# Optimization experiments

Measured on AMD Instinct MI355X. Metric: run time of the kernel, lower is better.

## Reference

```python
import jax, jax.numpy as jnp
import numpy as np

NUM_HEADS = 16


def setup_inputs() -> dict:
    key = jax.random.key(0)
    k1, k2, k3 = jax.random.split(key, 3)
    x = jax.random.normal(k1, (2, 2048, 1024), dtype=jnp.float32)
    w_qkv = jax.random.normal(k2, (3072, 1024), dtype=jnp.float32) * 0.02
    b_qkv = jax.random.normal(k3, (3072,), dtype=jnp.float32) * 0.02
    return {"x": x, "w_qkv": w_qkv, "b_qkv": b_qkv}


def reference(x, w_qkv, b_qkv):
    b, s, _ = x.shape
    d_model = w_qkv.shape[0] // 3
    head_dim = d_model // NUM_HEADS
    # fused QKV projection (torch Linear: x @ W^T + b)
    qkv = x @ w_qkv.T + b_qkv                      # [b, s, 3*d_model]
    qkv = qkv.reshape(b, s, NUM_HEADS, 3 * head_dim)
    qkv = jnp.transpose(qkv, (0, 2, 1, 3))          # [b, h, s, 3*hd]
    q, k, v = jnp.split(qkv, 3, axis=-1)            # each [b, h, s, hd]
    scale = 1.0 / np.sqrt(head_dim).astype(np.float32)
    scores = jnp.einsum("bhqd,bhkd->bhqk", q, k) * scale
    attn = jax.nn.softmax(scores, axis=-1)
    values = jnp.einsum("bhqk,bhkd->bhqd", attn, v)  # [b, h, s, hd]
    # Faithful to source: reshape WITHOUT permuting heads back (head-interleaved)
    return values.reshape(b, s, d_model)
```

## Files before the change

### kernel.cpp

```cpp
#include <hip/hip_runtime.h>
#include <cstdint>

typedef unsigned short ushort_t;

#define M_ROWS 4096
#define N_COLS 3072
#define K_DIM  1024
#define S_LEN  2048
#define NHEADS 16
#define HDIM   64
#define QSCALE 0.1803368801111204f

typedef __bf16 bf16_t;
typedef bf16_t  bf16x8  __attribute__((ext_vector_type(8)));
typedef short   shortx4 __attribute__((ext_vector_type(4)));
typedef float   floatx4 __attribute__((ext_vector_type(4)));
typedef ushort_t ushortx4 __attribute__((ext_vector_type(4)));

union U32x2S4 { unsigned u[2]; shortx4 s; };

__device__ __forceinline__ unsigned short f2bf(float f) {
  unsigned u = __float_as_uint(f);
  u += 0x7FFFu + ((u >> 16) & 1u);
  return (unsigned short)(u >> 16);
}

__device__ __forceinline__ unsigned pkbf(float a, float b) {
  unsigned ua = __float_as_uint(a) + 0x8000u;
  unsigned ub = __float_as_uint(b) + 0x8000u;
  return __builtin_amdgcn_perm(ub, ua, 0x07060302u);
}

__device__ __forceinline__ unsigned cvtpk(float a, float b) {
#if __has_builtin(__builtin_amdgcn_cvt_pk_bf16_f32)
  auto t = __builtin_amdgcn_cvt_pk_bf16_f32(a, b);
  unsigned r;
  __builtin_memcpy(&r, &t, 4);
  return r;
#else
  return pkbf(a, b);
#endif
}

__device__ __forceinline__ float fexp2(float x) {
#if __has_builtin(__builtin_amdgcn_exp2f)
  return __builtin_amdgcn_exp2f(x);
#else
  float r; asm volatile("v_exp_f32 %0, %1\n\ts_nop 1" : "=v"(r) : "v"(x)); return r;
#endif
}

__device__ __forceinline__ void gload_lds16(const void* g, void* l) {
  __builtin_amdgcn_global_load_lds(
      (const __attribute__((address_space(1))) unsigned int*)g,
      (__attribute__((address_space(3))) unsigned int*)l,
      16, 0, 0);
}

__global__ __launch_bounds__(256) void cvt_bf16_kernel(
    const float* __restrict__ x, const float* __restrict__ w,
    ushort_t* __restrict__ Xb, ushort_t* __restrict__ Wb) {
  const int NX8 = (M_ROWS * K_DIM) / 8;
  int i = blockIdx.x * 256 + threadIdx.x;
  const float4* src;
  ushort_t* dst;
  int idx;
  if (i < NX8) { src = (const float4*)x; dst = Xb; idx = i; }
  else         { src = (const float4*)w; dst = Wb; idx = i - NX8; }
  float4 a = src[2 * idx];
  float4 b = src[2 * idx + 1];
  uint4 o;
  o.x = cvtpk(a.x, a.y);
  o.y = cvtpk(a.z, a.w);
  o.z = cvtpk(b.x, b.y);
  o.w = cvtpk(b.z, b.w);
  *(uint4*)(dst + 8 * (size_t)idx) = o;
}

__global__ __launch_bounds__(256) void qkv_gemm_kernel(
    const ushort_t* __restrict__ Xb, const ushort_t* __restrict__ Wb,
    const float* __restrict__ bias,
    ushort_t* __restrict__ Qb, ushort_t* __restrict__ Kb, ushort_t* __restrict__ Vb) {
  __shared__ ushort_t As[128 * 64];
  __shared__ ushort_t Bs[128 * 64];
  const int tid = threadIdx.x;
  const int l = tid & 63, w = tid >> 6;
  const int quad = l >> 4, lj = l & 15;
  const int m0 = blockIdx.y * 128, n0 = blockIdx.x * 128;
  const int wm = (w & 1) * 64, wn = (w >> 1) * 64;

  floatx4 acc[4][4] = {};

  const int srow = w * 32 + (l >> 3);
  const int scol = ((l & 7) ^ (l >> 3)) * 8;
  const ushort_t* gA = Xb + (size_t)(m0 + srow) * K_DIM + scol;
  const ushort_t* gB = Wb + (size_t)(n0 + srow) * K_DIM + scol;
  ushort_t* lA = As + (w * 32) * 64;
  ushort_t* lB = Bs + (w * 32) * 64;

  const int swr = lj & 7;

  for (int k0 = 0; k0 < K_DIM; k0 += 64) {
    __syncthreads();
#pragma unroll
    for (int c = 0; c < 4; ++c) {
      gload_lds16(gA + (size_t)(c * 8) * K_DIM + k0, lA + c * 8 * 64);
      gload_lds16(gB + (size_t)(c * 8) * K_DIM + k0, lB + c * 8 * 64);
    }
    __syncthreads();
#pragma unroll
    for (int kk = 0; kk < 2; ++kk) {
      const int ch = ((kk * 4 + quad) ^ swr) * 8;
      bf16x8 aF[4], bF[4];
#pragma unroll
      for (int i = 0; i < 4; ++i)
        aF[i] = *(const bf16x8*)(As + (wm + i * 16 + lj) * 64 + ch);
#pragma unroll
      for (int j = 0; j < 4; ++j)
        bF[j] = *(const bf16x8*)(Bs + (wn + j * 16 + lj) * 64 + ch);
#pragma unroll
      for (int i = 0; i < 4; ++i)
#pragma unroll
        for (int j = 0; j < 4; ++j)
          acc[i][j] = __builtin_amdgcn_mfma_f32_16x16x32_bf16(aF[i], bF[j], acc[i][j], 0, 0, 0);
    }
  }

#pragma unroll
  for (int j = 0; j < 4; ++j) {
    const int n = n0 + wn + j * 16 + lj;
    const int h = n / 192;
    const int r = n - h * 192;
    const int seg = r >> 6;
    const int d = r & 63;
    const float bv = bias[n];
    ushort_t* dst = (seg == 0) ? Qb : (seg == 1) ? Kb : Vb;
    const float scl = (seg == 0) ? QSCALE : 1.0f;
    const size_t base = (size_t)h * S_LEN * HDIM + d;
#pragma unroll
    for (int i = 0; i < 4; ++i) {
#pragma unroll
      for (int rg = 0; rg < 4; ++rg) {
        const int m = m0 + wm + i * 16 + quad * 4 + rg;
        const int bi = m >> 11;
        const int si = m & 2047;
        dst[base + ((size_t)bi * NHEADS * S_LEN + si) * HDIM] =
            f2bf((acc[i][j][rg] + bv) * scl);
      }
    }
  }
}

__global__ __launch_bounds__(512, 4) void attn_kernel(
    const ushort_t* __restrict__ Qb, const ushort_t* __restrict__ Kb,
    const ushort_t* __restrict__ Vb, float* __restrict__ out) {
  __shared__ ushort_t Ks[128 * 64];
  __shared__ ushort_t Vs[64 * 140];
  const int tid = threadIdx.x;
  const int l = tid & 63, w = tid >> 6;
  const int quad = l >> 4, lj = l & 15;
  const int bh = blockIdx.x >> 4;
  const int qt = blockIdx.x & 15;
  const int q0 = qt * 128 + w * 16;
  const size_t headoff = (size_t)bh * S_LEN * HDIM;

  bf16x8 qF[2];
#pragma unroll
  for (int kk = 0; kk < 2; ++kk)
    qF[kk] = *(const bf16x8*)(Qb + headoff + (size_t)(q0 + lj) * HDIM +
                              kk * 32 + quad * 8);

  floatx4 accO[4] = {};
  float l_runA = 0.f, l_runB = 0.f;

  const int kr = tid >> 3;
  const int kc = ((tid & 7) ^ (kr & 7)) * 8;
  const ushort_t* gK = Kb + headoff + (size_t)kr * HDIM + kc;
  ushort_t* lK = Ks + tid * 8;

  const int dq = tid & 15;
  const int spw = tid >> 4;
  const ushort_t* gV = Vb + headoff + dq * 4;
  unsigned* Vs32 = (unsigned*)Vs;
  const int swz = (dq >> 2) << 1;

  const int swk = lj & 7;

  for (int kb = 0; kb < 16; ++kb) {
    const int kv0 = kb * 128;
    __syncthreads();
#pragma unroll
    for (int c = 0; c < 2; ++c)
      gload_lds16(gK + (size_t)(kv0 + c * 64) * HDIM, lK + c * 64 * 64);
#pragma unroll
    for (int R = 0; R < 2; ++R) {
      const int sp = R * 32 + spw;
      const ushort_t* g = gV + (size_t)(kv0 + 2 * sp) * HDIM;
      const uint2 v0 = *(const uint2*)g;
      const uint2 v1 = *(const uint2*)(g + HDIM);
      unsigned o0 = __builtin_amdgcn_perm(v1.x, v0.x, 0x05040100u);
      unsigned o1 = __builtin_amdgcn_perm(v1.x, v0.x, 0x07060302u);
      unsigned o2 = __builtin_amdgcn_perm(v1.y, v0.y, 0x05040100u);
      unsigned o3 = __builtin_amdgcn_perm(v1.y, v0.y, 0x07060302u);
      const int sp2 = sp ^ swz;
      Vs32[(4 * dq + 0) * 70 + sp2] = o0;
      Vs32[(4 * dq + 1) * 70 + sp2] = o1;
      Vs32[(4 * dq + 2) * 70 + sp2] = o2;
      Vs32[(4 * dq + 3) * 70 + sp2] = o3;
    }
    __syncthreads();

    floatx4 accST[8];
#pragma unroll
    for (int c = 0; c < 8; ++c) {
      const ushort_t* krow = Ks + (c * 16 + lj) * 64;
      bf16x8 kF0 = *(const bf16x8*)(krow + ((quad ^ swk) * 8));
      bf16x8 kF1 = *(const bf16x8*)(krow + (((quad ^ swk) ^ 4) * 8));
      floatx4 z = {0.f, 0.f, 0.f, 0.f};
      z = __builtin_amdgcn_mfma_f32_16x16x32_bf16(kF0, qF[0], z, 0, 0, 0);
      accST[c] = __builtin_amdgcn_mfma_f32_16x16x32_bf16(kF1, qF[1], z, 0, 0, 0);
    }

    shortx4 aP[8];
    float lsA = 0.f, lsB = 0.f;
#pragma unroll
    for (int c = 0; c < 8; ++c) {
      float p0 = fexp2(accST[c][0]);
      float p1 = fexp2(accST[c][1]);
      float p2 = fexp2(accST[c][2]);
      float p3 = fexp2(accST[c][3]);
      lsA += p0 + p1;
      lsB += p2 + p3;
      U32x2S4 t;
      t.u[0] = cvtpk(p0, p1);
      t.u[1] = cvtpk(p2, p3);
      aP[c] = t.s;
    }
    l_runA += lsA;
    l_runB += lsB;

#pragma unroll
    for (int dt = 0; dt < 4; ++dt) {
      const ushort_t* vp = Vs + (dt * 16 + lj) * 140 + (quad ^ dt) * 4;
#pragma unroll
      for (int c = 0; c < 8; ++c) {
        shortx4 vF = *(const shortx4*)(vp + c * 16);
        accO[dt] = __builtin_amdgcn_mfma_f32_16x16x16bf16_1k(aP[c], vF, accO[dt], 0, 0, 0);
      }
    }
  }

  {
    float ls = l_runA + l_runB;
    ls += __shfl_xor(ls, 16, 64);
    ls += __shfl_xor(ls, 32, 64);
    const float inv = 1.0f / ls;
    const int sbase = (l & 48) | (quad * 4);
    float iv[4];
    iv[0] = __shfl(inv, sbase + 0, 64);
    iv[1] = __shfl(inv, sbase + 1, 64);
    iv[2] = __shfl(inv, sbase + 2, 64);
    iv[3] = __shfl(inv, sbase + 3, 64);
#pragma unroll
    for (int dt = 0; dt < 4; ++dt) {
#pragma unroll
      for (int rg = 0; rg < 4; ++rg) {
        const int q = q0 + quad * 4 + rg;
        out[headoff + (size_t)q * HDIM + dt * 16 + lj] = accO[dt][rg] * iv[rg];
      }
    }
  }
}

extern "C" void kernel_launch(void* const* d_in, const int* in_sizes, int n_in,
                              void* d_out, int out_size, void* d_ws, size_t ws_size,
                              hipStream_t stream) {
  (void)in_sizes; (void)n_in; (void)out_size; (void)ws_size;
  const float* x  = (const float*)d_in[0];
  const float* wq = (const float*)d_in[1];
  const float* bq = (const float*)d_in[2];
  float* out = (float*)d_out;

  char* ws = (char*)d_ws;
  ushort_t* Qb = (ushort_t*)(ws);
  ushort_t* Kb = (ushort_t*)(ws + 8388608);
  ushort_t* Vb = (ushort_t*)(ws + 16777216);
  ushort_t* Xb = (ushort_t*)(ws + 25165824);
  ushort_t* Wb = (ushort_t*)(ws + 33554432);

  cvt_bf16_kernel<<<3584, 256, 0, stream>>>(x, wq, Xb, Wb);
  qkv_gemm_kernel<<<dim3(N_COLS / 128, M_ROWS / 128), 256, 0, stream>>>(Xb, Wb, bq, Qb, Kb, Vb);
  attn_kernel<<<512, 512, 0, stream>>>(Qb, Kb, Vb, out);
}
```

Baseline: 162.3 us.

## Load K fragments directly from global and remap block order for L2 locality

The attention kernel no longer stages K tiles in shared memory. Each lane loads its K fragments straight from global memory into registers, and the QK^T MFMA is fused with the exp/pack loop. The barrier now sits after the score computation, so the V stores to LDS overlap with the K loads and MFMAs. Block indices are also permuted so consecutive blocks land on different heads/q-tiles, which changes L2 reuse. In exchange, each of the 8 waves fetches K redundantly from global/L2 instead of once per block, which adds cache traffic.

```diff
diff --git a/kernel.cpp b/kernel.cpp
--- a/kernel.cpp
+++ b/kernel.cpp
@@ -154,13 +154,13 @@
 __global__ __launch_bounds__(512, 4) void attn_kernel(
     const ushort_t* __restrict__ Qb, const ushort_t* __restrict__ Kb,
     const ushort_t* __restrict__ Vb, float* __restrict__ out) {
-  __shared__ ushort_t Ks[128 * 64];
   __shared__ ushort_t Vs[64 * 140];
   const int tid = threadIdx.x;
   const int l = tid & 63, w = tid >> 6;
   const int quad = l >> 4, lj = l & 15;
-  const int bh = blockIdx.x >> 4;
-  const int qt = blockIdx.x & 15;
+  const int id = (blockIdx.x & 7) * 64 + (blockIdx.x >> 3);
+  const int bh = id >> 4;
+  const int qt = id & 15;
   const int q0 = qt * 128 + w * 16;
   const size_t headoff = (size_t)bh * S_LEN * HDIM;
 
@@ -172,11 +172,6 @@
 
   floatx4 accO[4] = {};
   float l_runA = 0.f, l_runB = 0.f;
-
-  const int kr = tid >> 3;
-  const int kc = ((tid & 7) ^ (kr & 7)) * 8;
-  const ushort_t* gK = Kb + headoff + (size_t)kr * HDIM + kc;
-  ushort_t* lK = Ks + tid * 8;
 
   const int dq = tid & 15;
   const int spw = tid >> 4;
@@ -184,14 +179,12 @@
   unsigned* Vs32 = (unsigned*)Vs;
   const int swz = (dq >> 2) << 1;
 
-  const int swk = lj & 7;
+  const ushort_t* gK = Kb + headoff + (size_t)lj * HDIM + quad * 8;
 
   for (int kb = 0; kb < 16; ++kb) {
     const int kv0 = kb * 128;
     __syncthreads();
-#pragma unroll
-    for (int c = 0; c < 2; ++c)
-      gload_lds16(gK + (size_t)(kv0 + c * 64) * HDIM, lK + c * 64 * 64);
+
 #pragma unroll
     for (int R = 0; R < 2; ++R) {
       const int sp = R * 32 + spw;
@@ -208,27 +201,22 @@
       Vs32[(4 * dq + 2) * 70 + sp2] = o2;
       Vs32[(4 * dq + 3) * 70 + sp2] = o3;
     }
-    __syncthreads();
-
-    floatx4 accST[8];
+
+    shortx4 aP[8];
+    float lsA = 0.f, lsB = 0.f;
+    const ushort_t* gKt = gK + (size_t)kv0 * HDIM;
 #pragma unroll
     for (int c = 0; c < 8; ++c) {
-      const ushort_t* krow = Ks + (c * 16 + lj) * 64;
-      bf16x8 kF0 = *(const bf16x8*)(krow + ((quad ^ swk) * 8));
-      bf16x8 kF1 = *(const bf16x8*)(krow + (((quad ^ swk) ^ 4) * 8));
+      const ushort_t* krow = gKt + (size_t)(c * 16) * HDIM;
+      bf16x8 kF0 = *(const bf16x8*)(krow);
+      bf16x8 kF1 = *(const bf16x8*)(krow + 32);
       floatx4 z = {0.f, 0.f, 0.f, 0.f};
       z = __builtin_amdgcn_mfma_f32_16x16x32_bf16(kF0, qF[0], z, 0, 0, 0);
-      accST[c] = __builtin_amdgcn_mfma_f32_16x16x32_bf16(kF1, qF[1], z, 0, 0, 0);
-    }
-
-    shortx4 aP[8];
-    float lsA = 0.f, lsB = 0.f;
-#pragma unroll
-    for (int c = 0; c < 8; ++c) {
-      float p0 = fexp2(accST[c][0]);
-      float p1 = fexp2(accST[c][1]);
-      float p2 = fexp2(accST[c][2]);
-      float p3 = fexp2(accST[c][3]);
+      floatx4 st = __builtin_amdgcn_mfma_f32_16x16x32_bf16(kF1, qF[1], z, 0, 0, 0);
+      float p0 = fexp2(st[0]);
+      float p1 = fexp2(st[1]);
+      float p2 = fexp2(st[2]);
+      float p3 = fexp2(st[3]);
       lsA += p0 + p1;
       lsB += p2 + p3;
       U32x2S4 t;
@@ -238,6 +226,7 @@
     }
     l_runA += lsA;
     l_runB += lsB;
+    __syncthreads();
 
 #pragma unroll
     for (int dt = 0; dt < 4; ++dt) {
```

Measured after the change: 240.6 us. 1.48x slower.

## Split attention KV range across two wave halves with LDS merge, double grid

Applied to the files above, without the earlier changes.

Each block now handles 64 query rows instead of 128. Its two halves of four waves each process opposite halves of the KV sequence, and the partial outputs and row sums are merged through LDS at the end. The grid doubles to 1024 blocks and is remapped so consecutive blocks spread across heads, which raises parallelism and may improve L2 locality. In exchange, each KV tile is loaded for half as many queries, so K/V traffic per query doubles. LDS use also doubles and an extra merge pass is added.

```diff
diff --git a/kernel.cpp b/kernel.cpp
--- a/kernel.cpp
+++ b/kernel.cpp
@@ -154,14 +154,17 @@
 __global__ __launch_bounds__(512, 4) void attn_kernel(
     const ushort_t* __restrict__ Qb, const ushort_t* __restrict__ Kb,
     const ushort_t* __restrict__ Vb, float* __restrict__ out) {
-  __shared__ ushort_t Ks[128 * 64];
-  __shared__ ushort_t Vs[64 * 140];
+  __shared__ ushort_t Ks[2][128 * 64];
+  __shared__ ushort_t Vs[2][64 * 140];
   const int tid = threadIdx.x;
   const int l = tid & 63, w = tid >> 6;
   const int quad = l >> 4, lj = l & 15;
-  const int bh = blockIdx.x >> 4;
-  const int qt = blockIdx.x & 15;
-  const int q0 = qt * 128 + w * 16;
+  const int half = w >> 2;
+  const int qg = w & 3;
+  const int id = (blockIdx.x & 7) * 128 + (blockIdx.x >> 3);
+  const int bh = id >> 5;
+  const int qt = id & 31;
+  const int q0 = qt * 64 + qg * 16;
   const size_t headoff = (size_t)bh * S_LEN * HDIM;
 
   bf16x8 qF[2];
@@ -176,26 +179,25 @@
   const int kr = tid >> 3;
   const int kc = ((tid & 7) ^ (kr & 7)) * 8;
   const ushort_t* gK = Kb + headoff + (size_t)kr * HDIM + kc;
-  ushort_t* lK = Ks + tid * 8;
 
   const int dq = tid & 15;
   const int spw = tid >> 4;
   const ushort_t* gV = Vb + headoff + dq * 4;
-  unsigned* Vs32 = (unsigned*)Vs;
   const int swz = (dq >> 2) << 1;
 
   const int swk = lj & 7;
 
-  for (int kb = 0; kb < 16; ++kb) {
-    const int kv0 = kb * 128;
-    __syncthreads();
+  auto STAGE = [&](int s, int tile) {
+    const int kv = tile * 128;
 #pragma unroll
     for (int c = 0; c < 2; ++c)
-      gload_lds16(gK + (size_t)(kv0 + c * 64) * HDIM, lK + c * 64 * 64);
+      gload_lds16(gK + (size_t)(kv + c * 64) * HDIM,
+                  &Ks[s][0] + tid * 8 + c * 64 * 64);
+    unsigned* vdst = (unsigned*)&Vs[s][0];
 #pragma unroll
     for (int R = 0; R < 2; ++R) {
       const int sp = R * 32 + spw;
-      const ushort_t* g = gV + (size_t)(kv0 + 2 * sp) * HDIM;
+      const ushort_t* g = gV + (size_t)(kv + 2 * sp) * HDIM;
       const uint2 v0 = *(const uint2*)g;
       const uint2 v1 = *(const uint2*)(g + HDIM);
       unsigned o0 = __builtin_amdgcn_perm(v1.x, v0.x, 0x05040100u);
@@ -203,17 +205,25 @@
       unsigned o2 = __builtin_amdgcn_perm(v1.y, v0.y, 0x05040100u);
       unsigned o3 = __builtin_amdgcn_perm(v1.y, v0.y, 0x07060302u);
       const int sp2 = sp ^ swz;
-      Vs32[(4 * dq + 0) * 70 + sp2] = o0;
-      Vs32[(4 * dq + 1) * 70 + sp2] = o1;
-      Vs32[(4 * dq + 2) * 70 + sp2] = o2;
-      Vs32[(4 * dq + 3) * 70 + sp2] = o3;
-    }
-    __syncthreads();
-
+      vdst[(4 * dq + 0) * 70 + sp2] = o0;
+      vdst[(4 * dq + 1) * 70 + sp2] = o1;
+      vdst[(4 * dq + 2) * 70 + sp2] = o2;
+      vdst[(4 * dq + 3) * 70 + sp2] = o3;
+    }
+  };
+
+  STAGE(0, 0);
+  STAGE(1, 8);
+  __syncthreads();
+
+  const ushort_t* Kc = &Ks[half][0];
+  const ushort_t* Vc = &Vs[half][0];
+
+  for (int r = 0; r < 8; ++r) {
     floatx4 accST[8];
 #pragma unroll
     for (int c = 0; c < 8; ++c) {
-      const ushort_t* krow = Ks + (c * 16 + lj) * 64;
+      const ushort_t* krow = Kc + (c * 16 + lj) * 64;
       bf16x8 kF0 = *(const bf16x8*)(krow + ((quad ^ swk) * 8));
       bf16x8 kF1 = *(const bf16x8*)(krow + (((quad ^ swk) ^ 4) * 8));
       floatx4 z = {0.f, 0.f, 0.f, 0.f};
@@ -241,17 +251,35 @@
 
 #pragma unroll
     for (int dt = 0; dt < 4; ++dt) {
-      const ushort_t* vp = Vs + (dt * 16 + lj) * 140 + (quad ^ dt) * 4;
+      const ushort_t* vp = Vc + (dt * 16 + lj) * 140 + (quad ^ dt) * 4;
 #pragma unroll
       for (int c = 0; c < 8; ++c) {
         shortx4 vF = *(const shortx4*)(vp + c * 16);
         accO[dt] = __builtin_amdgcn_mfma_f32_16x16x16bf16_1k(aP[c], vF, accO[dt], 0, 0, 0);
       }
     }
-  }
-
-  {
-    float ls = l_runA + l_runB;
+
+    __syncthreads();
+    if (r < 7) {
+      STAGE(0, r + 1);
+      STAGE(1, r + 9);
+    }
+    __syncthreads();
+  }
+
+  float* mrg = (float*)&Ks[0][0];
+  float* lbf = (float*)&Vs[0][0];
+  if (half == 1) {
+#pragma unroll
+    for (int dt = 0; dt < 4; ++dt)
+#pragma unroll
+      for (int rg = 0; rg < 4; ++rg)
+        mrg[(qg * 16 + dt * 4 + rg) * 64 + l] = accO[dt][rg];
+    lbf[qg * 64 + l] = l_runA + l_runB;
+  }
+  __syncthreads();
+  if (half == 0) {
+    float ls = l_runA + l_runB + lbf[qg * 64 + l];
     ls += __shfl_xor(ls, 16, 64);
     ls += __shfl_xor(ls, 32, 64);
     const float inv = 1.0f / ls;
@@ -266,7 +294,8 @@
 #pragma unroll
       for (int rg = 0; rg < 4; ++rg) {
         const int q = q0 + quad * 4 + rg;
-        out[headoff + (size_t)q * HDIM + dt * 16 + lj] = accO[dt][rg] * iv[rg];
+        const float o = accO[dt][rg] + mrg[(qg * 16 + dt * 4 + rg) * 64 + l];
+        out[headoff + (size_t)q * HDIM + dt * 16 + lj] = o * iv[rg];
       }
     }
   }
@@ -290,5 +319,5 @@
 
   cvt_bf16_kernel<<<3584, 256, 0, stream>>>(x, wq, Xb, Wb);
   qkv_gemm_kernel<<<dim3(N_COLS / 128, M_ROWS / 128), 256, 0, stream>>>(Xb, Wb, bq, Qb, Kb, Vb);
-  attn_kernel<<<512, 512, 0, stream>>>(Qb, Kb, Vb, out);
-}
+  attn_kernel<<<1024, 512, 0, stream>>>(Qb, Kb, Vb, out);
+}
```

Measured after the change: 171.5 us. 1.06x slower.
